# Performance work log

Measured on AMD Instinct MI355X. Metric: run time of the kernel, lower is better.

## Reference

```python
import jax, jax.numpy as jnp
import numpy as np

B, T, D = 2, 2048, 1024
NH, NKV, HD = 16, 4, 64
BASE, TSL, QGI = 10000.0, 1024, 1.5
EPS = 1.1920929e-07  # torch.finfo(float32).eps used by F.rms_norm default


def _rope_cos_sin(seq_len, rd):
    # Rotary.forward with self.rd == head_dim (Attn sets rd=0 -> full rotation)
    if seq_len > TSL:  # NTK-style base rescale branch
        nb = BASE * (seq_len / TSL) ** (rd / (rd - 2))
    else:
        nb = BASE
    inv = 1.0 / nb ** (jnp.arange(0, rd, 2, dtype=jnp.float32) / rd)
    fr = jnp.arange(seq_len, dtype=jnp.float32)[:, None] * inv[None, :]
    return jnp.cos(fr)[None, :, None, :], jnp.sin(fr)[None, :, None, :]


def _apply_rope(x, cos, sin):
    h = x.shape[-1] // 2
    x1, x2 = x[..., :h], x[..., h:]
    return jnp.concatenate([x1 * cos + x2 * sin, -x1 * sin + x2 * cos], axis=-1)


def _rms_norm(x):
    return x * jax.lax.rsqrt(jnp.mean(x * x, axis=-1, keepdims=True) + EPS)


def setup_inputs() -> dict:
    key = jax.random.key(0)
    ks = jax.random.split(key, 8)
    s = jnp.float32(0.02)
    return {
        "x": jax.random.normal(ks[0], (B, T, D), jnp.float32),
        "qw": jax.random.normal(ks[1], (NH * HD, D), jnp.float32) * s,
        "kw": jax.random.normal(ks[2], (NKV * HD, D), jnp.float32) * s,
        "vw": jax.random.normal(ks[3], (NKV * HD, D), jnp.float32) * s,
        "ow": jax.random.normal(ks[4], (D, D), jnp.float32) * s,
        "ve": jax.random.normal(ks[5], (B, T, NKV * HD), jnp.float32) * s,
        "v0": jax.random.normal(ks[6], (B, T, NKV, HD), jnp.float32) * s,
        "q_gain": jnp.full((NH,), QGI, jnp.float32),
        "vr_lambda": jnp.array([0.5, 0.5], jnp.float32),
        "gate_w": jnp.zeros((NH, D), jnp.float32),      # nn.init.zeros_
        "gate_b": jnp.full((NH,), 4.0, jnp.float32),    # nn.init.constant_(4.0)
    }


def reference(x, qw, kw, vw, ow, ve, v0, q_gain, vr_lambda, gate_w, gate_b):
    # projections
    q = (x @ qw.T).reshape(B, T, NH, HD)
    k = (x @ kw.T).reshape(B, T, NKV, HD)
    v = (x @ vw.T + ve).reshape(B, T, NKV, HD)
    raw_v = v  # returned when vr=True
    v = vr_lambda[0] * v0 + vr_lambda[1] * v  # value residual
    # qk rms-norm + rope (full head dim since self.rd == 0) + per-head q gain
    q = _rms_norm(q)
    k = _rms_norm(k)
    cos, sin = _rope_cos_sin(T, HD)
    q = _apply_rope(q, cos, sin)
    k = _apply_rope(k, cos, sin)
    q = q * q_gain[None, None, :, None]
    # causal GQA attention (nh query heads share nkv kv heads)
    G = NH // NKV
    qg = q.reshape(B, T, NKV, G, HD)
    scale = 1.0 / np.sqrt(HD).astype(np.float32)
    scores = jnp.einsum('bqhgd,bkhd->bhgqk', qg, k) * scale  # [B,NKV,G,T,T]
    causal = jnp.tril(jnp.ones((T, T), bool))
    scores = jnp.where(causal[None, None, None], scores, jnp.finfo(scores.dtype).min)
    p = jax.nn.softmax(scores, axis=-1)
    y = jnp.einsum('bhgqk,bkhd->bqhgd', p, v).reshape(B, T, NH, HD)
    # gated attention output
    gate = jax.nn.sigmoid(x @ gate_w.T + gate_b)  # [B,T,NH]
    y = y * gate[..., None]
    out = y.reshape(B, T, D) @ ow.T
    return out, raw_v
```

## Files before the change

kernel.cpp:

```cpp
#include <hip/hip_runtime.h>
#include <math.h>

#define BB 2
#define TT 2048
#define DD 1024
#define NH 16
#define NKV 4
#define HD 64
#define EPSF 1.1920929e-07f
#define LOG2_NB 14.319970444065578
#define SCALE_LOG2E 0.18033688011112042f
#define FIXMAX 17.5f

typedef __attribute__((ext_vector_type(8))) short bf16x8;
typedef __attribute__((ext_vector_type(4))) float f32x4;

__device__ inline short f2bf(float f) {
    unsigned u = __builtin_bit_cast(unsigned, f);
    unsigned r = (u + 0x7fffu + ((u >> 16) & 1u)) >> 16;
    return (short)r;
}
__device__ inline float bf2f(short s) {
    unsigned u = ((unsigned)(unsigned short)s) << 16;
    return __builtin_bit_cast(float, u);
}
__device__ inline unsigned cvt_pk_bf16(float a, float b) {
    unsigned r;
    asm("v_cvt_pk_bf16_f32 %0, %1, %2" : "=v"(r) : "v"(a), "v"(b));
    return r;
}

__global__ __launch_bounds__(256) void conv_all(
    const float* __restrict__ x, const float* __restrict__ qw,
    const float* __restrict__ kw, const float* __restrict__ vw,
    const float* __restrict__ ow,
    short* __restrict__ x16, short* __restrict__ wb16, short* __restrict__ ow16)
{
    int i = blockIdx.x * 256 + threadIdx.x;
    const float* src; short* dst; int j;
    if (i < 1048576)      { src = x;  dst = x16;            j = i; }
    else if (i < 1310720) { src = qw; dst = wb16;           j = i - 1048576; }
    else if (i < 1376256) { src = kw; dst = wb16 + 1048576; j = i - 1310720; }
    else if (i < 1441792) { src = vw; dst = wb16 + 1310720; j = i - 1376256; }
    else                  { src = ow; dst = ow16;           j = i - 1441792; }
    float4 v = ((const float4*)src)[j];
    short4 o;
    o.x = f2bf(v.x); o.y = f2bf(v.y); o.z = f2bf(v.z); o.w = f2bf(v.w);
    ((short4*)dst)[j] = o;
}

#define GSTAGE(buf, k0, Abase, Bbase)                                                   \
{                                                                                       \
    _Pragma("unroll")                                                                   \
    for (int i_ = 0; i_ < 2; i_++) {                                                    \
        int off = w*2048 + i_*1024;                      \
        int g = (off >> 4) + lane;                                   \
        int row = g >> 2, c = g & 3;                                                    \
        int cg = c ^ (row & 3);                                        \
        const short* ga = (Abase) + (size_t)(m0 + row)*1024 + (k0) + cg*8;              \
        __builtin_amdgcn_global_load_lds(                                               \
            (const __attribute__((address_space(1))) void*)ga,                          \
            (__attribute__((address_space(3))) void*)((char*)&As[buf][0] + off), 16, 0, 0); \
        const short* gb = (Bbase) + (size_t)(n0 + row)*1024 + (k0) + cg*8;              \
        __builtin_amdgcn_global_load_lds(                                               \
            (const __attribute__((address_space(1))) void*)gb,                          \
            (__attribute__((address_space(3))) void*)((char*)&Bs[buf][0] + off), 16, 0, 0); \
    }                                                                                   \
}

#define GEMM_MAIN_LOOP(kbeg, kend, Abase, Bbase)                                        \
    GSTAGE(0, (kbeg), (Abase), (Bbase));                                                \
    __syncthreads();                                                                    \
    for (int k0 = (kbeg); k0 < (kend); k0 += 32) {                                      \
        int cur = ((k0 - (kbeg)) >> 5) & 1;                                             \
        bf16x8 af[4], bfr[4];                                                           \
        _Pragma("unroll")                                                               \
        for (int tm = 0; tm < 4; tm++) {                                                \
            int row = wy*64 + tm*16 + lc;                                               \
            af[tm] = *(const bf16x8*)(&As[cur][0] + row*32 + ((quad*8) ^ ((row&3)*8))); \
        }                                                                               \
        _Pragma("unroll")                                                               \
        for (int tn = 0; tn < 4; tn++) {                                                \
            int row = wx*64 + tn*16 + lc;                                               \
            bfr[tn] = *(const bf16x8*)(&Bs[cur][0] + row*32 + ((quad*8) ^ ((row&3)*8))); \
        }                                                                               \
        if (k0 + 32 < (kend)) GSTAGE(cur ^ 1, k0 + 32, (Abase), (Bbase));               \
        _Pragma("unroll")                                                               \
        for (int tm = 0; tm < 4; tm++)                                                  \
            _Pragma("unroll")                                                           \
            for (int tn = 0; tn < 4; tn++)                                              \
                acc[tm][tn] = __builtin_amdgcn_mfma_f32_16x16x32_bf16(af[tm], bfr[tn], acc[tm][tn], 0, 0, 0); \
        __syncthreads();                                                                \
    }

__global__ __launch_bounds__(256, 3) void gemm_qkv_fused(
    const short* __restrict__ A, const short* __restrict__ Bmat,
    const float* __restrict__ ve, const float* __restrict__ v0,
    const float* __restrict__ q_gain, const float* __restrict__ vr_lambda,
    short* __restrict__ qbh, short* __restrict__ kbh, short* __restrict__ vb,
    float* __restrict__ rawv)
{
    __shared__ short As[2][128*32];
    __shared__ short Bs[2][128*32];
    int tid = threadIdx.x;
    int w = tid >> 6, lane = tid & 63;
    int quad = lane >> 4, lc = lane & 15;
    int wy = w >> 1, wx = w & 1;
    int m0 = blockIdx.y * 128, n0 = blockIdx.x * 128;

    f32x4 acc[4][4];
    #pragma unroll
    for (int i = 0; i < 4; i++)
        #pragma unroll
        for (int j = 0; j < 4; j++) acc[i][j] = (f32x4){0.f,0.f,0.f,0.f};

    GEMM_MAIN_LOOP(0, 1024, A, Bmat);

    int hc = n0 + wx*64;
    if (hc < 1280) {
        bool isq = (hc < 1024);
        int h = isq ? (hc >> 6) : ((hc - 1024) >> 6);
        float gsc = isq ? (q_gain[h] * SCALE_LOG2E) : 1.0f;
        short* dst = isq ? qbh : kbh;
        int nhh = isq ? 16 : 4;
        float inv0 = (float)exp2((double)lc * (-LOG2_NB / 32.0));
        float inv1 = (float)exp2((double)(lc + 16) * (-LOG2_NB / 32.0));
        #pragma unroll
        for (int tm = 0; tm < 4; tm++) {
            #pragma unroll
            for (int r = 0; r < 4; r++) {
                int m = m0 + wy*64 + tm*16 + quad*4 + r;
                int b = m >> 11, t = m & (TT - 1);
                float a0 = acc[tm][0][r], a1 = acc[tm][1][r];
                float a2 = acc[tm][2][r], a3 = acc[tm][3][r];
                float ss = a0*a0 + a1*a1 + a2*a2 + a3*a3;
                ss += __shfl_xor(ss, 1);
                ss += __shfl_xor(ss, 2);
                ss += __shfl_xor(ss, 4);
                ss += __shfl_xor(ss, 8);
                float rn = rsqrtf(ss * (1.0f/64.0f) + EPSF);
                a0 *= rn; a1 *= rn; a2 *= rn; a3 *= rn;
                float sn0, cs0, sn1, cs1;
                sincosf((float)t * inv0, &sn0, &cs0);
                sincosf((float)t * inv1, &sn1, &cs1);
                float o0 = a0*cs0 + a2*sn0;
                float o1 = a1*cs1 + a3*sn1;
                float o2 = a2*cs0 - a0*sn0;
                float o3 = a3*cs1 - a1*sn1;
                size_t base = (((size_t)(b*nhh + h))*2048 + t)*64 + lc;
                dst[base +  0] = f2bf(o0 * gsc);
                dst[base + 16] = f2bf(o1 * gsc);
                dst[base + 32] = f2bf(o2 * gsc);
                dst[base + 48] = f2bf(o3 * gsc);
            }
        }
    } else {
        int vh = (hc - 1280) >> 6;
        float l0 = vr_lambda[0], l1 = vr_lambda[1];
        #pragma unroll
        for (int tm = 0; tm < 4; tm++) {
            #pragma unroll
            for (int r = 0; r < 4; r++) {
                int m = m0 + wy*64 + tm*16 + quad*4 + r;
                size_t off = (size_t)m*256 + vh*64 + lc;
                #pragma unroll
                for (int tn = 0; tn < 4; tn++) {
                    float val = acc[tm][tn][r] + ve[off + tn*16];
                    rawv[off + tn*16] = val;
                    vb[off + tn*16] = f2bf(l0 * v0[off + tn*16] + l1 * val);
                }
            }
        }
    }
}

__global__ __launch_bounds__(256, 4) void gemm_mfma(
    const short* __restrict__ A, const short* __restrict__ Bmat,
    float* __restrict__ C, int ldc, int klen)
{
    __shared__ short As[2][128*32];
    __shared__ short Bs[2][128*32];
    int tid = threadIdx.x;
    int w = tid >> 6, lane = tid & 63;
    int quad = lane >> 4, lc = lane & 15;
    int wy = w >> 1, wx = w & 1;
    int m0 = blockIdx.y * 128, n0 = blockIdx.x * 128;

    f32x4 acc[4][4];
    #pragma unroll
    for (int i = 0; i < 4; i++)
        #pragma unroll
        for (int j = 0; j < 4; j++) acc[i][j] = (f32x4){0.f,0.f,0.f,0.f};

    GEMM_MAIN_LOOP(0, klen, A, Bmat);

    #pragma unroll
    for (int tm = 0; tm < 4; tm++)
        #pragma unroll
        for (int r = 0; r < 4; r++) {
            int m = m0 + wy*64 + tm*16 + quad*4 + r;
            #pragma unroll
            for (int tn = 0; tn < 4; tn++) {
                int n = n0 + wx*64 + tn*16 + lc;
                C[(size_t)m*ldc + n] = acc[tm][tn][r];
            }
        }
}

__global__ __launch_bounds__(256) void transpose_v(
    const short* __restrict__ vb, short* __restrict__ vtb)
{
    __shared__ short tile[64][72];
    int bk = blockIdx.x;
    int tt = blockIdx.y;
    int b = bk >> 2, kvh = bk & 3;
    int tid = threadIdx.x;
    int t4 = tid >> 4;
    int d4 = (tid & 15) * 4;
    #pragma unroll
    for (int i = 0; i < 4; i++) {
        int t = t4 + i*16;
        const short* src = vb + (((size_t)(b*2048 + tt*64 + t)*4 + kvh)*64 + d4);
        *(short4*)&tile[t][d4] = *(const short4*)src;
    }
    __syncthreads();
    #pragma unroll
    for (int i = 0; i < 4; i++) {
        int d = t4 + i*16;
        int t0 = d4;
        short4 o;
        o.x = tile[t0+0][d]; o.y = tile[t0+1][d];
        o.z = tile[t0+2][d]; o.w = tile[t0+3][d];
        *(short4*)&vtb[((size_t)(bk*64 + d))*2048 + tt*64 + t0] = o;
    }
}

__global__ __launch_bounds__(256) void gate_kernel(
    const short* __restrict__ x16, const float* __restrict__ gw,
    const float* __restrict__ gb, float* __restrict__ gate)
{
    __shared__ float xs[1024];
    int row = blockIdx.x;
    int tid = threadIdx.x;
    short4 sv = *(const short4*)&x16[(size_t)row*1024 + tid*4];
    xs[tid*4+0] = bf2f(sv.x); xs[tid*4+1] = bf2f(sv.y);
    xs[tid*4+2] = bf2f(sv.z); xs[tid*4+3] = bf2f(sv.w);
    __syncthreads();
    int wave = tid >> 6, lane = tid & 63;
    for (int h = wave; h < 16; h += 4) {
        const float* w = gw + (size_t)h * 1024;
        float s = 0.f;
        #pragma unroll
        for (int i = 0; i < 16; i++) s += xs[lane + 64*i] * w[lane + 64*i];
        #pragma unroll
        for (int off = 32; off; off >>= 1) s += __shfl_xor(s, off);
        if (lane == 0) gate[(size_t)row*16 + h] = 1.0f / (1.0f + __expf(-(s + gb[h])));
    }
}

__global__ __launch_bounds__(256, 4) void flash_mfma(
    const short* __restrict__ qbh, const short* __restrict__ kbh,
    const short* __restrict__ vtb, const float* __restrict__ gate,
    short* __restrict__ y16)
{
    __shared__ short Ks[2][64*64];
    __shared__ short Vt[2][64*64];
    __shared__ short Ps[4][16*64];

    int bh = blockIdx.x;
    int b = bh >> 4, h = bh & 15, kvh = h >> 2;
    int qt = 31 - blockIdx.y;
    int tid = threadIdx.x;
    int w = tid >> 6, lane = tid & 63;
    int quad = lane >> 4, lc = lane & 15;

    const short* qbase = qbh + (((size_t)bh)*2048 + qt*64 + w*16 + lc)*64;
    bf16x8 qf0 = *(const bf16x8*)(qbase + quad*8);
    bf16x8 qf1 = *(const bf16x8*)(qbase + 32 + quad*8);

    f32x4 o[4];
    #pragma unroll
    for (int i = 0; i < 4; i++) o[i] = (f32x4){0.f,0.f,0.f,0.f};
    f32x4 l4 = (f32x4){0.f,0.f,0.f,0.f};
    const bf16x8 ones = {(short)0x3F80,(short)0x3F80,(short)0x3F80,(short)0x3F80,
                         (short)0x3F80,(short)0x3F80,(short)0x3F80,(short)0x3F80};

    const size_t kbase = ((size_t)(b*4 + kvh))*2048*64;
    const size_t vbase = ((size_t)(b*4 + kvh))*64*2048;

    #define STAGE(buf, kt)                                                              \
    {                                                                                   \
        _Pragma("unroll")                                                               \
        for (int i = 0; i < 2; i++) {                                                   \
            int off = w*2048 + i*1024;                                                  \
            int g = (off >> 4) + lane;                                                  \
            int row = g >> 3, c = g & 7;                                                \
            int cg = c ^ (row & 7);                                                     \
            const short* gk = kbh + kbase + (size_t)((kt)*64 + row)*64 + cg*8;          \
            __builtin_amdgcn_global_load_lds(                                           \
                (const __attribute__((address_space(1))) void*)gk,                      \
                (__attribute__((address_space(3))) void*)((char*)Ks[buf] + off), 16, 0, 0); \
            const short* gv = vtb + vbase + (size_t)row*2048 + (kt)*64 + cg*8;          \
            __builtin_amdgcn_global_load_lds(                                           \
                (const __attribute__((address_space(1))) void*)gv,                      \
                (__attribute__((address_space(3))) void*)((char*)Vt[buf] + off), 16, 0, 0); \
        }                                                                               \
    }

    STAGE(0, 0);
    __syncthreads();

    short* ps = Ps[w];

    for (int kt = 0; kt <= qt; kt++) {
        int cur = kt & 1;
        bool diag = (kt == qt);

        bf16x8 kf0[4], kf1[4], vf0[4], vf1[4];
        #pragma unroll
        for (int kn = 0; kn < 4; kn++) {
            int row = kn*16 + lc;
            int sw = (row & 7) * 8;
            const short* kr = Ks[cur] + row*64;
            kf0[kn] = *(const bf16x8*)(kr + ((quad*8) ^ sw));
            kf1[kn] = *(const bf16x8*)(kr + ((quad*8 + 32) ^ sw));
            const short* vr = Vt[cur] + row*64;
            vf0[kn] = *(const bf16x8*)(vr + ((quad*8) ^ sw));
            vf1[kn] = *(const bf16x8*)(vr + ((quad*8 + 32) ^ sw));
        }
        if (kt < qt) STAGE(cur ^ 1, kt + 1);

        f32x4 s4[4];
        #pragma unroll
        for (int kn = 0; kn < 4; kn++) {
            f32x4 acc = (f32x4){0.f,0.f,0.f,0.f};
            acc = __builtin_amdgcn_mfma_f32_16x16x32_bf16(kf0[kn], qf0, acc, 0, 0, 0);
            acc = __builtin_amdgcn_mfma_f32_16x16x32_bf16(kf1[kn], qf1, acc, 0, 0, 0);
            s4[kn] = acc;
        }

        #pragma unroll
        for (int kn = 0; kn < 4; kn++) {
            float p0 = __builtin_amdgcn_exp2f(s4[kn][0] - FIXMAX);
            float p1 = __builtin_amdgcn_exp2f(s4[kn][1] - FIXMAX);
            float p2 = __builtin_amdgcn_exp2f(s4[kn][2] - FIXMAX);
            float p3 = __builtin_amdgcn_exp2f(s4[kn][3] - FIXMAX);
            if (diag) {
                int keyb = kn*16 + quad*4, qv = w*16 + lc;
                if (keyb + 0 > qv) p0 = 0.f;
                if (keyb + 1 > qv) p1 = 0.f;
                if (keyb + 2 > qv) p2 = 0.f;
                if (keyb + 3 > qv) p3 = 0.f;
            }
            int c = kn*4 + quad;
            int cs = c ^ ((lc & 7) << 1);
            int2 pk;
            pk.x = (int)cvt_pk_bf16(p0, p1);
            pk.y = (int)cvt_pk_bf16(p2, p3);
            *(int2*)(ps + lc*64 + cs*4) = pk;
        }
        __asm__ volatile("s_waitcnt lgkmcnt(0)" ::: "memory");
        int u0 = (0*4 + quad) ^ (lc & 7);
        int u1 = (1*4 + quad) ^ (lc & 7);
        bf16x8 pf0 = *(const bf16x8*)(ps + lc*64 + u0*8);
        bf16x8 pf1 = *(const bf16x8*)(ps + lc*64 + u1*8);

        #pragma unroll
        for (int dn = 0; dn < 4; dn++) {
            o[dn] = __builtin_amdgcn_mfma_f32_16x16x32_bf16(pf0, vf0[dn], o[dn], 0, 0, 0);
            o[dn] = __builtin_amdgcn_mfma_f32_16x16x32_bf16(pf1, vf1[dn], o[dn], 0, 0, 0);
        }
        l4 = __builtin_amdgcn_mfma_f32_16x16x32_bf16(pf0, ones, l4, 0, 0, 0);
        l4 = __builtin_amdgcn_mfma_f32_16x16x32_bf16(pf1, ones, l4, 0, 0, 0);
        __syncthreads();
    }

    #pragma unroll
    for (int r = 0; r < 4; r++) {
        int row = b*2048 + qt*64 + w*16 + quad*4 + r;
        float g = gate[(size_t)row*16 + h] / l4[r];
        #pragma unroll
        for (int dn = 0; dn < 4; dn++)
            y16[(size_t)row*1024 + h*64 + dn*16 + lc] = f2bf(o[dn][r] * g);
    }
}

extern "C" void kernel_launch(void* const* d_in, const int* in_sizes, int n_in,
                              void* d_out, int out_size, void* d_ws, size_t ws_size,
                              hipStream_t stream) {
    (void)in_sizes; (void)n_in; (void)out_size; (void)ws_size;
    const float* x  = (const float*)d_in[0];
    const float* qw = (const float*)d_in[1];
    const float* kw = (const float*)d_in[2];
    const float* vw = (const float*)d_in[3];
    const float* ow = (const float*)d_in[4];
    const float* ve = (const float*)d_in[5];
    const float* v0 = (const float*)d_in[6];
    const float* qg = (const float*)d_in[7];
    const float* vl = (const float*)d_in[8];
    const float* gw = (const float*)d_in[9];
    const float* gb = (const float*)d_in[10];

    float* out  = (float*)d_out;
    float* rawv = out + (size_t)BB*TT*DD;

    float* p    = (float*)d_ws;
    short* x16  = (short*)p;        p += 2097152;
    short* wb16 = (short*)p;        p += 786432;
    short* ow16 = (short*)p;        p += 524288;
    short* qbh  = (short*)p;        p += 2097152;
    short* kbh  = (short*)p;        p += 524288;
    short* vtb  = (short*)p;        p += 524288;
    short* vb   = (short*)p;        p += 524288;
    float* gt   = p;                p += 65536;
    short* y16  = (short*)p;

    conv_all<<<6656, 256, 0, stream>>>(x, qw, kw, vw, ow, x16, wb16, ow16);
    gemm_qkv_fused<<<dim3(12, 32), 256, 0, stream>>>(x16, wb16, ve, v0, qg, vl,
                                                     qbh, kbh, vb, rawv);
    transpose_v<<<dim3(8, 32), 256, 0, stream>>>(vb, vtb);
    gate_kernel<<<4096, 256, 0, stream>>>(x16, gw, gb, gt);
    flash_mfma<<<dim3(32, 32), 256, 0, stream>>>(qbh, kbh, vtb, gt, y16);
    gemm_mfma<<<dim3(8, 32), 256, 0, stream>>>(y16, ow16, out, 1024, 1024);
}
```

Measured before the change: 199.8 us.

## Fuse gate projection and V transpose into QKV GEMM epilogue

The gate weights are converted to bf16 and appended as an extra zero-padded 128-column tile of the QKV weight matrix, so the gate logits and sigmoid come out of the fused GEMM. The V epilogue now transposes through shared memory and writes the transposed V layout directly. This removes the separate transpose_v and gate_kernel launches and the intermediate vb buffer. The cost is an extra GEMM column block that is mostly zero padding, and the gate dot product now uses bf16 weights instead of fp32.

```diff
diff --git a/kernel.cpp b/kernel.cpp
--- a/kernel.cpp
+++ b/kernel.cpp
@@ -33,16 +33,21 @@
 __global__ __launch_bounds__(256) void conv_all(
     const float* __restrict__ x, const float* __restrict__ qw,
     const float* __restrict__ kw, const float* __restrict__ vw,
-    const float* __restrict__ ow,
+    const float* __restrict__ ow, const float* __restrict__ gw,
     short* __restrict__ x16, short* __restrict__ wb16, short* __restrict__ ow16)
 {
     int i = blockIdx.x * 256 + threadIdx.x;
+    if (i >= 1708032) {
+        ((short4*)(wb16 + 1552*1024))[i - 1708032] = (short4){0,0,0,0};
+        return;
+    }
     const float* src; short* dst; int j;
     if (i < 1048576)      { src = x;  dst = x16;            j = i; }
     else if (i < 1310720) { src = qw; dst = wb16;           j = i - 1048576; }
     else if (i < 1376256) { src = kw; dst = wb16 + 1048576; j = i - 1310720; }
     else if (i < 1441792) { src = vw; dst = wb16 + 1310720; j = i - 1376256; }
-    else                  { src = ow; dst = ow16;           j = i - 1441792; }
+    else if (i < 1703936) { src = ow; dst = ow16;           j = i - 1441792; }
+    else                  { src = gw; dst = wb16 + 1572864; j = i - 1703936; }
     float4 v = ((const float4*)src)[j];
     short4 o;
     o.x = f2bf(v.x); o.y = f2bf(v.y); o.z = f2bf(v.z); o.w = f2bf(v.w);
@@ -97,7 +102,8 @@
     const short* __restrict__ A, const short* __restrict__ Bmat,
     const float* __restrict__ ve, const float* __restrict__ v0,
     const float* __restrict__ q_gain, const float* __restrict__ vr_lambda,
-    short* __restrict__ qbh, short* __restrict__ kbh, short* __restrict__ vb,
+    const float* __restrict__ gb_, float* __restrict__ gate,
+    short* __restrict__ qbh, short* __restrict__ kbh, short* __restrict__ vtb,
     float* __restrict__ rawv)
 {
     __shared__ short As[2][128*32];
@@ -154,23 +160,45 @@
                 dst[base + 48] = f2bf(o3 * gsc);
             }
         }
-    } else {
-        int vh = (hc - 1280) >> 6;
+    } else if (hc < 1536) {
+        int kvh = (hc - 1280) >> 6;
         float l0 = vr_lambda[0], l1 = vr_lambda[1];
+        short* lbase = (w < 2) ? &As[w][0] : &Bs[w - 2][0];
         #pragma unroll
         for (int tm = 0; tm < 4; tm++) {
             #pragma unroll
             for (int r = 0; r < 4; r++) {
                 int m = m0 + wy*64 + tm*16 + quad*4 + r;
-                size_t off = (size_t)m*256 + vh*64 + lc;
+                int tl = tm*16 + quad*4 + r;
+                size_t off = (size_t)m*256 + kvh*64 + lc;
                 #pragma unroll
                 for (int tn = 0; tn < 4; tn++) {
+                    int d = tn*16 + lc;
                     float val = acc[tm][tn][r] + ve[off + tn*16];
                     rawv[off + tn*16] = val;
-                    vb[off + tn*16] = f2bf(l0 * v0[off + tn*16] + l1 * val);
+                    lbase[d*64 + (tl ^ ((d & 7) * 8))] = f2bf(l0 * v0[off + tn*16] + l1 * val);
                 }
             }
         }
+        int b = m0 >> 11;
+        int t0g = (m0 & 2047) + wy*64;
+        short* vdst = vtb + (size_t)(b*4 + kvh)*64*2048;
+        #pragma unroll
+        for (int j = 0; j < 16; j++) {
+            int d = quad + j*4;
+            int tc = lc*4;
+            short4 vv = *(const short4*)&lbase[d*64 + (tc ^ ((d & 7) * 8))];
+            *(short4*)&vdst[(size_t)d*2048 + t0g + tc] = vv;
+        }
+    } else if (hc == 1536) {
+        #pragma unroll
+        for (int tm = 0; tm < 4; tm++)
+            #pragma unroll
+            for (int r = 0; r < 4; r++) {
+                int m = m0 + wy*64 + tm*16 + quad*4 + r;
+                float lg = acc[tm][0][r] + gb_[lc];
+                gate[(size_t)m*16 + lc] = 1.0f / (1.0f + __expf(-lg));
+            }
     }
 }
 
@@ -205,57 +233,6 @@
                 C[(size_t)m*ldc + n] = acc[tm][tn][r];
             }
         }
-}
-
-__global__ __launch_bounds__(256) void transpose_v(
-    const short* __restrict__ vb, short* __restrict__ vtb)
-{
-    __shared__ short tile[64][72];
-    int bk = blockIdx.x;
-    int tt = blockIdx.y;
-    int b = bk >> 2, kvh = bk & 3;
-    int tid = threadIdx.x;
-    int t4 = tid >> 4;
-    int d4 = (tid & 15) * 4;
-    #pragma unroll
-    for (int i = 0; i < 4; i++) {
-        int t = t4 + i*16;
-        const short* src = vb + (((size_t)(b*2048 + tt*64 + t)*4 + kvh)*64 + d4);
-        *(short4*)&tile[t][d4] = *(const short4*)src;
-    }
-    __syncthreads();
-    #pragma unroll
-    for (int i = 0; i < 4; i++) {
-        int d = t4 + i*16;
-        int t0 = d4;
-        short4 o;
-        o.x = tile[t0+0][d]; o.y = tile[t0+1][d];
-        o.z = tile[t0+2][d]; o.w = tile[t0+3][d];
-        *(short4*)&vtb[((size_t)(bk*64 + d))*2048 + tt*64 + t0] = o;
-    }
-}
-
-__global__ __launch_bounds__(256) void gate_kernel(
-    const short* __restrict__ x16, const float* __restrict__ gw,
-    const float* __restrict__ gb, float* __restrict__ gate)
-{
-    __shared__ float xs[1024];
-    int row = blockIdx.x;
-    int tid = threadIdx.x;
-    short4 sv = *(const short4*)&x16[(size_t)row*1024 + tid*4];
-    xs[tid*4+0] = bf2f(sv.x); xs[tid*4+1] = bf2f(sv.y);
-    xs[tid*4+2] = bf2f(sv.z); xs[tid*4+3] = bf2f(sv.w);
-    __syncthreads();
-    int wave = tid >> 6, lane = tid & 63;
-    for (int h = wave; h < 16; h += 4) {
-        const float* w = gw + (size_t)h * 1024;
-        float s = 0.f;
-        #pragma unroll
-        for (int i = 0; i < 16; i++) s += xs[lane + 64*i] * w[lane + 64*i];
-        #pragma unroll
-        for (int off = 32; off; off >>= 1) s += __shfl_xor(s, off);
-        if (lane == 0) gate[(size_t)row*16 + h] = 1.0f / (1.0f + __expf(-(s + gb[h])));
-    }
 }
 
 __global__ __launch_bounds__(256, 4) void flash_mfma(
@@ -406,20 +383,17 @@
 
     float* p    = (float*)d_ws;
     short* x16  = (short*)p;        p += 2097152;
-    short* wb16 = (short*)p;        p += 786432;
+    short* wb16 = (short*)p;        p += 851968;
     short* ow16 = (short*)p;        p += 524288;
     short* qbh  = (short*)p;        p += 2097152;
     short* kbh  = (short*)p;        p += 524288;
     short* vtb  = (short*)p;        p += 524288;
-    short* vb   = (short*)p;        p += 524288;
     float* gt   = p;                p += 65536;
     short* y16  = (short*)p;
 
-    conv_all<<<6656, 256, 0, stream>>>(x, qw, kw, vw, ow, x16, wb16, ow16);
-    gemm_qkv_fused<<<dim3(12, 32), 256, 0, stream>>>(x16, wb16, ve, v0, qg, vl,
-                                                     qbh, kbh, vb, rawv);
-    transpose_v<<<dim3(8, 32), 256, 0, stream>>>(vb, vtb);
-    gate_kernel<<<4096, 256, 0, stream>>>(x16, gw, gb, gt);
+    conv_all<<<6784, 256, 0, stream>>>(x, qw, kw, vw, ow, gw, x16, wb16, ow16);
+    gemm_qkv_fused<<<dim3(13, 32), 256, 0, stream>>>(x16, wb16, ve, v0, qg, vl,
+                                                     gb, gt, qbh, kbh, vtb, rawv);
     flash_mfma<<<dim3(32, 32), 256, 0, stream>>>(qbh, kbh, vtb, gt, y16);
     gemm_mfma<<<dim3(8, 32), 256, 0, stream>>>(y16, ow16, out, 1024, 1024);
 }
```

Result: faster. 186.1 us (-6.9%).
